# Kernel tuning notes

Hardware: AMD Instinct MI355X
Metric: run time of the kernel (lower is better)

The kernel has to match this reference:

```python
import jax, jax.numpy as jnp
import numpy as np

N, V, E = 65536, 2048, 1024
TEMPERATURE = 0.5
EPS = 1e-10
LOG_PARAM_Q = -2.995732273553991


def _l2_normalize(x, axis):
    # matches torch F.normalize(p=2): x / max(||x||, 1e-12)
    n = jnp.sqrt(jnp.sum(x * x, axis=axis, keepdims=True))
    return x / jnp.maximum(n, 1e-12)


def setup_inputs() -> dict:
    key = jax.random.key(0)
    k1, k2, k3 = jax.random.split(key, 3)
    z = jax.random.normal(k1, (N, E), dtype=jnp.float32)
    emb_weight = jax.random.normal(k2, (V, E), dtype=jnp.float32)
    U = jax.random.uniform(k3, (N, V), dtype=jnp.float32)
    return {"z": z, "emb_weight": emb_weight, "U": U}


def reference(z, emb_weight, U):
    kappa_q = jnp.exp(jnp.float32(LOG_PARAM_Q)) + jnp.float32(1.0)
    zn = _l2_normalize(z, axis=1)              # [N, E]
    emb = _l2_normalize(emb_weight, axis=1)    # [V, E]
    # logit = -distances = kappa_q * z @ emb.T
    logit = kappa_q * jnp.matmul(zn, emb.T)    # [N, V]
    # gumbel-softmax sample (training branch)
    g = -jnp.log(-jnp.log(U + EPS) + EPS)
    tokens = jax.nn.softmax((logit + g) / TEMPERATURE, axis=-1)  # [N, V]
    z_q = jnp.matmul(tokens, emb)              # [N, E]
    return (tokens, z_q)
```

## Files before the change

### kernel.cpp

```cpp
#include <hip/hip_runtime.h>
#include <hip/hip_bf16.h>
#include <stdint.h>

typedef short bf16x8 __attribute__((ext_vector_type(8)));
typedef float floatx4 __attribute__((ext_vector_type(4)));

#define N_ROWS 65536
#define V_DIM 2048
#define E_DIM 1024

__device__ __forceinline__ short f2bf(float x) {
  union { float f; uint32_t u; } c; c.f = x;
  uint32_t r = (c.u + 0x7FFFu + ((c.u >> 16) & 1u)) >> 16;
  return (short)(uint16_t)r;
}
__device__ __forceinline__ float bf16f(short b) {
  union { uint32_t u; float f; } c; c.u = ((uint32_t)(uint16_t)b) << 16;
  return c.f;
}

__device__ __forceinline__ float wave_sum(float v) {
#pragma unroll
  for (int o = 32; o > 0; o >>= 1) v += __shfl_xor(v, o);
  return v;
}
__device__ __forceinline__ float wave_max(float v) {
#pragma unroll
  for (int o = 32; o > 0; o >>= 1) v = fmaxf(v, __shfl_xor(v, o));
  return v;
}

__device__ __forceinline__ void gll16(const short* g, short* l) {
  __builtin_amdgcn_global_load_lds(
      (const __attribute__((address_space(1))) void*)g,
      (__attribute__((address_space(3))) void*)l, 16, 0, 0);
}

#define FRAG(base, R, c) \
  (*(const bf16x8*)((const char*)(base) + ((R) << 7) + (((((c) >> 3) ^ ((R) & 7))) << 4)))

__global__ __launch_bounds__(256) void k_norm_emb(const float* __restrict__ W,
                                                  short* __restrict__ embn,
                                                  short* __restrict__ embnT) {
  const int v = blockIdx.x;
  const int t = threadIdx.x;
  const int w = t >> 6, l = t & 63;
  const float4 val = *(const float4*)&W[(size_t)v * E_DIM + t * 4];
  float ss = val.x * val.x + val.y * val.y + val.z * val.z + val.w * val.w;
  ss = wave_sum(ss);
  __shared__ float red[4];
  if (l == 0) red[w] = ss;
  __syncthreads();
  ss = red[0] + red[1] + red[2] + red[3];
  const float inv = 1.0f / fmaxf(sqrtf(ss), 1e-12f);
  short4 o;
  o.x = f2bf(val.x * inv);
  o.y = f2bf(val.y * inv);
  o.z = f2bf(val.z * inv);
  o.w = f2bf(val.w * inv);
  *(short4*)&embn[(size_t)v * E_DIM + t * 4] = o;
  embnT[(size_t)(t * 4 + 0) * V_DIM + v] = o.x;
  embnT[(size_t)(t * 4 + 1) * V_DIM + v] = o.y;
  embnT[(size_t)(t * 4 + 2) * V_DIM + v] = o.z;
  embnT[(size_t)(t * 4 + 3) * V_DIM + v] = o.w;
}

__global__ __launch_bounds__(256) void k_norm_z(const float* __restrict__ Z,
                                                short* __restrict__ zn) {
  const int w = threadIdx.x >> 6, l = threadIdx.x & 63;
  const int row = blockIdx.x * 4 + w;
  const float* zr = Z + (size_t)row * E_DIM;
  float4 v[4];
  float ss = 0.f;
#pragma unroll
  for (int i = 0; i < 4; ++i) {
    v[i] = *(const float4*)&zr[(i * 64 + l) * 4];
    ss += v[i].x * v[i].x + v[i].y * v[i].y + v[i].z * v[i].z + v[i].w * v[i].w;
  }
  ss = wave_sum(ss);
  const float SCALE = 2.0f * (expf(-2.995732273553991f) + 1.0f);
  const float inv = SCALE / fmaxf(sqrtf(ss), 1e-12f);
  short* zo = zn + (size_t)row * E_DIM;
#pragma unroll
  for (int i = 0; i < 4; ++i) {
    short4 o;
    o.x = f2bf(v[i].x * inv);
    o.y = f2bf(v[i].y * inv);
    o.z = f2bf(v[i].z * inv);
    o.w = f2bf(v[i].w * inv);
    *(short4*)&zo[(i * 64 + l) * 4] = o;
  }
}

template <int KDIM, int NBX, int EPI>
__global__ __launch_bounds__(512, 2) void k_gemm8(
    const short* __restrict__ A, const short* __restrict__ B,
    const float* __restrict__ U, short* __restrict__ Pb,
    float* __restrict__ partials, const float* __restrict__ invsum,
    float* __restrict__ C, int cpx) {
  __shared__ __align__(16) short Sm[65536];
  const int NT = KDIM / 32;
  const int tid = threadIdx.x;
  const int wv = tid >> 6, lane = tid & 63;
  const int lr = lane & 15, lh = lane >> 4;
  const int wr = wv >> 2, wc = wv & 3;
  const int d = blockIdx.x;
  const int L = (d & 7) * cpx + (d >> 3);
  const int by = L / NBX, bx = L % NBX;
  const int m0 = by * 256, n0 = bx * 256;
  const int sg = (((lane & 3) ^ ((lane >> 2) & 3) ^ ((lane >> 4) & 3)) << 3);
  const int srow = wv * 16 + (lane >> 2);
  const short* gA = A + (size_t)(m0 + srow) * KDIM + sg;
  const short* gB = B + (size_t)(n0 + srow) * KDIM + sg;
  const int fslot = lh ^ ((lr ^ (lr >> 2)) & 3);
  const int aoff = wr * 8192 + lr * 64 + fslot * 16;
  const int boff = wc * 4096 + lr * 64 + fslot * 16;

  bf16x8 af[4], afN[4], bfr[4];
  floatx4 acc[8][4] = {};

#define STAGE(KT)                                                                   \
  {                                                                                 \
    short* An_ = Sm + ((KT) & 3) * 8192;                                            \
    short* Bn_ = Sm + 32768 + ((KT) & 3) * 8192;                                    \
    const size_t kc_ = (size_t)(KT) * 32;                                           \
    gll16(gA + kc_, An_ + wv * 512);                                                \
    gll16(gA + (size_t)128 * KDIM + kc_, An_ + 4096 + wv * 512);                    \
    gll16(gB + kc_, Bn_ + wv * 512);                                                \
    gll16(gB + (size_t)128 * KDIM + kc_, Bn_ + 4096 + wv * 512);                    \
  }
#define RD_B(KT)                                                                    \
  {                                                                                 \
    const char* Bb_ = (const char*)Sm + 65536 + ((KT) & 3) * 16384;                 \
    _Pragma("unroll")                                                               \
    for (int n = 0; n < 4; ++n) bfr[n] = *(const bf16x8*)(Bb_ + boff + n * 1024);   \
  }
#define RD_ALO(KT)                                                                  \
  {                                                                                 \
    const char* Ab_ = (const char*)Sm + ((KT) & 3) * 16384;                         \
    _Pragma("unroll")                                                               \
    for (int i = 0; i < 4; ++i) af[i] = *(const bf16x8*)(Ab_ + aoff + i * 1024);    \
  }
#define RD_AHI(KT)                                                                  \
  {                                                                                 \
    const char* Ab_ = (const char*)Sm + ((KT) & 3) * 16384;                         \
    _Pragma("unroll")                                                               \
    for (int i = 0; i < 4; ++i)                                                     \
      afN[i] = *(const bf16x8*)(Ab_ + aoff + 4096 + i * 1024);                      \
  }
#define MF_LO                                                                       \
  __builtin_amdgcn_s_setprio(1);                                                    \
  _Pragma("unroll")                                                                 \
  for (int i = 0; i < 4; ++i) {                                                     \
    _Pragma("unroll")                                                               \
    for (int n = 0; n < 4; ++n)                                                     \
      acc[i][n] = __builtin_amdgcn_mfma_f32_16x16x32_bf16(af[i], bfr[n], acc[i][n], 0, 0, 0); \
  }                                                                                 \
  __builtin_amdgcn_s_setprio(0);
#define MF_HI                                                                       \
  __builtin_amdgcn_s_setprio(1);                                                    \
  _Pragma("unroll")                                                                 \
  for (int i = 0; i < 4; ++i) {                                                     \
    _Pragma("unroll")                                                               \
    for (int n = 0; n < 4; ++n)                                                     \
      acc[4 + i][n] = __builtin_amdgcn_mfma_f32_16x16x32_bf16(afN[i], bfr[n], acc[4 + i][n], 0, 0, 0); \
  }                                                                                 \
  __builtin_amdgcn_s_setprio(0);

  STAGE(0);
  STAGE(1);
  asm volatile("s_waitcnt vmcnt(4)" ::: "memory");
  __builtin_amdgcn_s_barrier();
  __builtin_amdgcn_sched_barrier(0);
  RD_B(0);
  RD_ALO(0);

#pragma unroll 2
  for (int kt = 0; kt < NT - 2; ++kt) {
    STAGE(kt + 2);
    RD_AHI(kt);
    MF_LO;
    MF_HI;
    asm volatile("s_waitcnt vmcnt(4)" ::: "memory");
    __builtin_amdgcn_s_barrier();
    __builtin_amdgcn_sched_barrier(0);
    RD_B(kt + 1);
    RD_ALO(kt + 1);
  }
  RD_AHI(NT - 2);
  MF_LO;
  MF_HI;
  asm volatile("s_waitcnt vmcnt(0)" ::: "memory");
  __builtin_amdgcn_s_barrier();
  __builtin_amdgcn_sched_barrier(0);
  RD_B(NT - 1);
  RD_ALO(NT - 1);
  RD_AHI(NT - 1);
  MF_LO;
  MF_HI;
#undef STAGE
#undef RD_B
#undef RD_ALO
#undef RD_AHI
#undef MF_LO
#undef MF_HI

  const int gr0 = m0 + wr * 128 + lh * 4;
  const int gc0 = n0 + wc * 64 + lr;
  if (EPI == 0) {
    float rs[8][4] = {};
#pragma unroll
    for (int m = 0; m < 8; ++m)
#pragma unroll
      for (int n = 0; n < 4; ++n) {
        const int col = gc0 + n * 16;
#pragma unroll
        for (int j = 0; j < 4; ++j) {
          const int row = gr0 + m * 16 + j;
          const size_t idx = (size_t)row * V_DIM + col;
          const float u = U[idx];
          const float e = __expf(acc[m][n][j] - 2.f * __logf(-__logf(u + 1e-10f) + 1e-10f));
          const short eb = f2bf(e);
          Pb[idx] = eb;
          rs[m][j] += bf16f(eb);
        }
      }
#pragma unroll
    for (int m = 0; m < 8; ++m)
#pragma unroll
      for (int j = 0; j < 4; ++j) {
        float s = rs[m][j];
        s += __shfl_xor(s, 1); s += __shfl_xor(s, 2);
        s += __shfl_xor(s, 4); s += __shfl_xor(s, 8);
        if (lr == 0)
          partials[(size_t)(gr0 + m * 16 + j) * 32 + bx * 4 + wc] = s;
      }
  } else {
#pragma unroll
    for (int m = 0; m < 8; ++m)
#pragma unroll
      for (int j = 0; j < 4; ++j) {
        const int row = gr0 + m * 16 + j;
        const float s = invsum[row];
#pragma unroll
        for (int n = 0; n < 4; ++n)
          C[(size_t)row * E_DIM + gc0 + n * 16] = acc[m][n][j] * s;
      }
  }
}

__global__ __launch_bounds__(256) void k_rowsum_inv(const float* __restrict__ partials,
                                                    float* __restrict__ invsum) {
  const int r = blockIdx.x * 256 + threadIdx.x;
  const float4* p = (const float4*)&partials[(size_t)r * 32];
  float s = 0.f;
#pragma unroll
  for (int i = 0; i < 8; ++i) { float4 v = p[i]; s += v.x + v.y + v.z + v.w; }
  invsum[r] = 1.f / s;
}

__global__ __launch_bounds__(256) void k_token_norm(const short* __restrict__ Pb,
                                                    const float* __restrict__ invsum,
                                                    float* __restrict__ tokens) {
  const size_t stride = (size_t)gridDim.x * 256 * 8;
  for (size_t i = ((size_t)blockIdx.x * 256 + threadIdx.x) * 8;
       i < (size_t)N_ROWS * V_DIM; i += stride) {
    const float s = invsum[i >> 11];
    const bf16x8 v = *(const bf16x8*)&Pb[i];
    float4 o0, o1;
    o0.x = bf16f(v[0]) * s; o0.y = bf16f(v[1]) * s;
    o0.z = bf16f(v[2]) * s; o0.w = bf16f(v[3]) * s;
    o1.x = bf16f(v[4]) * s; o1.y = bf16f(v[5]) * s;
    o1.z = bf16f(v[6]) * s; o1.w = bf16f(v[7]) * s;
    *(float4*)&tokens[i] = o0;
    *(float4*)&tokens[i + 4] = o1;
  }
}

__global__ __launch_bounds__(256) void k_gemm_nt(const short* __restrict__ A,
                                                 const short* __restrict__ B,
                                                 float* __restrict__ C,
                                                 int lda, int ldb, int ldc, int K) {
  __shared__ __align__(16) short As[128][64];
  __shared__ __align__(16) short Bs[128][64];
  const int t = threadIdx.x;
  const int w = t >> 6, l = t & 63;
  const int lr = l & 15, lh = l >> 4;
  const int m0 = blockIdx.y * 128, n0 = blockIdx.x * 128;
  const int wm = (w >> 1) * 64, wn = (w & 1) * 64;
  floatx4 acc[4][4] = {};
  for (int k0 = 0; k0 < K; k0 += 64) {
    __syncthreads();
#pragma unroll
    for (int i = 0; i < 4; ++i) {
      const int c = i * 256 + t;
      const int r = c >> 3, c8 = (c & 7) * 8;
      *(bf16x8*)&As[r][c8] = *(const bf16x8*)&A[(size_t)(m0 + r) * lda + k0 + c8];
      *(bf16x8*)&Bs[r][c8] = *(const bf16x8*)&B[(size_t)(n0 + r) * ldb + k0 + c8];
    }
    __syncthreads();
#pragma unroll
    for (int kk = 0; kk < 64; kk += 32) {
      bf16x8 af[4], bfr[4];
#pragma unroll
      for (int m = 0; m < 4; ++m) af[m] = *(const bf16x8*)&As[wm + m * 16 + lr][kk + lh * 8];
#pragma unroll
      for (int n = 0; n < 4; ++n) bfr[n] = *(const bf16x8*)&Bs[wn + n * 16 + lr][kk + lh * 8];
#pragma unroll
      for (int m = 0; m < 4; ++m)
#pragma unroll
        for (int n = 0; n < 4; ++n)
          acc[m][n] = __builtin_amdgcn_mfma_f32_16x16x32_bf16(af[m], bfr[n], acc[m][n], 0, 0, 0);
    }
  }
#pragma unroll
  for (int m = 0; m < 4; ++m)
#pragma unroll
    for (int n = 0; n < 4; ++n) {
      const int col = n0 + wn + n * 16 + lr;
#pragma unroll
      for (int j = 0; j < 4; ++j)
        C[(size_t)(m0 + wm + m * 16 + lh * 4 + j) * ldc + col] = acc[m][n][j];
    }
}

__global__ __launch_bounds__(256) void k_gemm_nt_f32a(const float* __restrict__ A,
                                                      const short* __restrict__ B,
                                                      float* __restrict__ C,
                                                      int lda, int ldb, int ldc, int K) {
  __shared__ __align__(16) short As[128][64];
  __shared__ __align__(16) short Bs[128][64];
  const int t = threadIdx.x;
  const int w = t >> 6, l = t & 63;
  const int lr = l & 15, lh = l >> 4;
  const int m0 = blockIdx.y * 128, n0 = blockIdx.x * 128;
  const int wm = (w >> 1) * 64, wn = (w & 1) * 64;
  floatx4 acc[4][4] = {};
  for (int k0 = 0; k0 < K; k0 += 64) {
    __syncthreads();
#pragma unroll
    for (int i = 0; i < 4; ++i) {
      const int c = i * 256 + t;
      const int r = c >> 3, c8 = (c & 7) * 8;
      const float4 a0 = *(const float4*)&A[(size_t)(m0 + r) * lda + k0 + c8];
      const float4 a1 = *(const float4*)&A[(size_t)(m0 + r) * lda + k0 + c8 + 4];
      bf16x8 va;
      va[0] = f2bf(a0.x); va[1] = f2bf(a0.y); va[2] = f2bf(a0.z); va[3] = f2bf(a0.w);
      va[4] = f2bf(a1.x); va[5] = f2bf(a1.y); va[6] = f2bf(a1.z); va[7] = f2bf(a1.w);
      *(bf16x8*)&As[r][c8] = va;
      *(bf16x8*)&Bs[r][c8] = *(const bf16x8*)&B[(size_t)(n0 + r) * ldb + k0 + c8];
    }
    __syncthreads();
#pragma unroll
    for (int kk = 0; kk < 64; kk += 32) {
      bf16x8 af[4], bfr[4];
#pragma unroll
      for (int m = 0; m < 4; ++m) af[m] = *(const bf16x8*)&As[wm + m * 16 + lr][kk + lh * 8];
#pragma unroll
      for (int n = 0; n < 4; ++n) bfr[n] = *(const bf16x8*)&Bs[wn + n * 16 + lr][kk + lh * 8];
#pragma unroll
      for (int m = 0; m < 4; ++m)
#pragma unroll
        for (int n = 0; n < 4; ++n)
          acc[m][n] = __builtin_amdgcn_mfma_f32_16x16x32_bf16(af[m], bfr[n], acc[m][n], 0, 0, 0);
    }
  }
#pragma unroll
  for (int m = 0; m < 4; ++m)
#pragma unroll
    for (int n = 0; n < 4; ++n) {
      const int col = n0 + wn + n * 16 + lr;
#pragma unroll
      for (int j = 0; j < 4; ++j)
        C[(size_t)(m0 + wm + m * 16 + lh * 4 + j) * ldc + col] = acc[m][n][j];
    }
}

__global__ __launch_bounds__(256) void k_gumbel_softmax(float* __restrict__ S,
                                                        const float* __restrict__ U) {
  const int t = threadIdx.x;
  const int w = t >> 6, l = t & 63;
  const size_t base = (size_t)blockIdx.x * V_DIM + t * 8;
  const float4 s0 = *(const float4*)&S[base];
  const float4 s1 = *(const float4*)&S[base + 4];
  const float4 u0 = *(const float4*)&U[base];
  const float4 u1 = *(const float4*)&U[base + 4];
  float x[8];
  x[0] = s0.x - 2.f * __logf(-__logf(u0.x + 1e-10f) + 1e-10f);
  x[1] = s0.y - 2.f * __logf(-__logf(u0.y + 1e-10f) + 1e-10f);
  x[2] = s0.z - 2.f * __logf(-__logf(u0.z + 1e-10f) + 1e-10f);
  x[3] = s0.w - 2.f * __logf(-__logf(u0.w + 1e-10f) + 1e-10f);
  x[4] = s1.x - 2.f * __logf(-__logf(u1.x + 1e-10f) + 1e-10f);
  x[5] = s1.y - 2.f * __logf(-__logf(u1.y + 1e-10f) + 1e-10f);
  x[6] = s1.z - 2.f * __logf(-__logf(u1.z + 1e-10f) + 1e-10f);
  x[7] = s1.w - 2.f * __logf(-__logf(u1.w + 1e-10f) + 1e-10f);
  float lm = x[0];
#pragma unroll
  for (int i = 1; i < 8; ++i) lm = fmaxf(lm, x[i]);
  lm = wave_max(lm);
  __shared__ float redA[4], redB[4];
  if (l == 0) redA[w] = lm;
  __syncthreads();
  const float m = fmaxf(fmaxf(redA[0], redA[1]), fmaxf(redA[2], redA[3]));
  float p[8];
  float ls = 0.f;
#pragma unroll
  for (int i = 0; i < 8; ++i) { p[i] = __expf(x[i] - m); ls += p[i]; }
  ls = wave_sum(ls);
  if (l == 0) redB[w] = ls;
  __syncthreads();
  const float inv = 1.0f / (redB[0] + redB[1] + redB[2] + redB[3]);
  float4 o0 = make_float4(p[0] * inv, p[1] * inv, p[2] * inv, p[3] * inv);
  float4 o1 = make_float4(p[4] * inv, p[5] * inv, p[6] * inv, p[7] * inv);
  *(float4*)&S[base] = o0;
  *(float4*)&S[base + 4] = o1;
}

extern "C" void kernel_launch(void* const* d_in, const int* in_sizes, int n_in,
                              void* d_out, int out_size, void* d_ws, size_t ws_size,
                              hipStream_t stream) {
  const float* z = (const float*)d_in[0];
  const float* W = (const float*)d_in[1];
  const float* U = (const float*)d_in[2];
  float* tokens = (float*)d_out;
  float* zq = tokens + (size_t)N_ROWS * V_DIM;
  short* zn = (short*)zq;

  short* embn = (short*)d_ws;
  short* embnT = embn + (size_t)V_DIM * E_DIM;

  const size_t NEED = (size_t)V_DIM * E_DIM * 2 * 2
                    + (size_t)N_ROWS * 32 * 4
                    + (size_t)N_ROWS * 4
                    + (size_t)N_ROWS * V_DIM * 2;

  k_norm_emb<<<V_DIM, 256, 0, stream>>>(W, embn, embnT);
  k_norm_z<<<N_ROWS / 4, 256, 0, stream>>>(z, zn);

  if (ws_size >= NEED) {
    float* partials = (float*)(embnT + (size_t)V_DIM * E_DIM);
    float* invsum = partials + (size_t)N_ROWS * 32;
    short* Pb = (short*)(invsum + N_ROWS);
    k_gemm8<E_DIM, 8, 0><<<2048, 512, 0, stream>>>(
        zn, embn, U, Pb, partials, nullptr, nullptr, 2048 / 8);
    k_rowsum_inv<<<N_ROWS / 256, 256, 0, stream>>>(partials, invsum);
    k_token_norm<<<2048, 256, 0, stream>>>(Pb, invsum, tokens);
    k_gemm8<V_DIM, 4, 1><<<1024, 512, 0, stream>>>(
        Pb, embnT, nullptr, nullptr, nullptr, invsum, zq, 1024 / 8);
  } else {
    k_gemm_nt<<<dim3(V_DIM / 128, N_ROWS / 128), 256, 0, stream>>>(
        zn, embn, tokens, E_DIM, E_DIM, V_DIM, E_DIM);
    k_gumbel_softmax<<<N_ROWS, 256, 0, stream>>>(tokens, U);
    k_gemm_nt_f32a<<<dim3(E_DIM / 128, N_ROWS / 128), 256, 0, stream>>>(
        tokens, embnT, zq, V_DIM, V_DIM, E_DIM, V_DIM);
  }
}
```

Measured before the change: 1.013 ms.

## Fuse token normalization into second GEMM and prefetch U for epilogue

```diff
diff --git a/kernel.cpp b/kernel.cpp
--- a/kernel.cpp
+++ b/kernel.cpp
@@ -97,7 +97,7 @@
     const short* __restrict__ A, const short* __restrict__ B,
     const float* __restrict__ U, short* __restrict__ Pb,
     float* __restrict__ partials, const float* __restrict__ invsum,
-    float* __restrict__ C, int cpx) {
+    float* __restrict__ C, float* __restrict__ tokens, int cpx) {
   __shared__ __align__(16) short Sm[65536];
   const int NT = KDIM / 32;
   const int tid = threadIdx.x;
@@ -116,8 +116,31 @@
   const int aoff = wr * 8192 + lr * 64 + fslot * 16;
   const int boff = wc * 4096 + lr * 64 + fslot * 16;
 
+  const int gr0 = m0 + wr * 128 + lh * 4;
+  const int gc0 = n0 + wc * 64 + lr;
+  const float* Ug = U + (size_t)gr0 * V_DIM + gc0;
+
+  float inv0 = 0.f, inv1 = 0.f;
+  if (EPI == 1) {
+    inv0 = invsum[m0 + srow];
+    inv1 = invsum[m0 + 128 + srow];
+  }
+
   bf16x8 af[4], afN[4], bfr[4];
   floatx4 acc[8][4] = {};
+  float u01[32], u23[32];
+
+#define UPREF(arr, P)                                                               \
+  {                                                                                 \
+    _Pragma("unroll")                                                               \
+    for (int mm = 0; mm < 2; ++mm)                                                  \
+      _Pragma("unroll")                                                             \
+      for (int n = 0; n < 4; ++n)                                                   \
+        _Pragma("unroll")                                                           \
+        for (int j = 0; j < 4; ++j)                                                 \
+          arr[mm * 16 + n * 4 + j] =                                                \
+              Ug[(size_t)(((2 * (P) + mm) * 16 + j)) * V_DIM + n * 16];             \
+  }
 
 #define STAGE(KT)                                                                   \
   {                                                                                 \
@@ -166,6 +189,26 @@
       acc[4 + i][n] = __builtin_amdgcn_mfma_f32_16x16x32_bf16(afN[i], bfr[n], acc[4 + i][n], 0, 0, 0); \
   }                                                                                 \
   __builtin_amdgcn_s_setprio(0);
+#define TOKW(KT)                                                                    \
+  if (EPI == 1 && ((KT) >> 4) == bx) {                                              \
+    const short* myA_ = Sm + ((KT) & 3) * 8192 + wv * 512 + lane * 8;               \
+    const bf16x8 v0_ = *(const bf16x8*)myA_;                                        \
+    const bf16x8 v1_ = *(const bf16x8*)(myA_ + 4096);                               \
+    const size_t c0_ = (size_t)(KT) * 32 + sg;                                      \
+    float4 a_, b_;                                                                  \
+    a_.x = bf16f(v0_[0]) * inv0; a_.y = bf16f(v0_[1]) * inv0;                       \
+    a_.z = bf16f(v0_[2]) * inv0; a_.w = bf16f(v0_[3]) * inv0;                       \
+    b_.x = bf16f(v0_[4]) * inv0; b_.y = bf16f(v0_[5]) * inv0;                       \
+    b_.z = bf16f(v0_[6]) * inv0; b_.w = bf16f(v0_[7]) * inv0;                       \
+    *(float4*)&tokens[(size_t)(m0 + srow) * KDIM + c0_] = a_;                       \
+    *(float4*)&tokens[(size_t)(m0 + srow) * KDIM + c0_ + 4] = b_;                   \
+    a_.x = bf16f(v1_[0]) * inv1; a_.y = bf16f(v1_[1]) * inv1;                       \
+    a_.z = bf16f(v1_[2]) * inv1; a_.w = bf16f(v1_[3]) * inv1;                       \
+    b_.x = bf16f(v1_[4]) * inv1; b_.y = bf16f(v1_[5]) * inv1;                       \
+    b_.z = bf16f(v1_[6]) * inv1; b_.w = bf16f(v1_[7]) * inv1;                       \
+    *(float4*)&tokens[(size_t)(m0 + 128 + srow) * KDIM + c0_] = a_;                 \
+    *(float4*)&tokens[(size_t)(m0 + 128 + srow) * KDIM + c0_ + 4] = b_;             \
+  }
 
   STAGE(0);
   STAGE(1);
@@ -177,10 +220,13 @@
 
 #pragma unroll 2
   for (int kt = 0; kt < NT - 2; ++kt) {
+    if (EPI == 0 && kt == NT - 6) UPREF(u01, 0);
+    if (EPI == 0 && kt == NT - 4) UPREF(u23, 1);
     STAGE(kt + 2);
     RD_AHI(kt);
     MF_LO;
     MF_HI;
+    TOKW(kt);
     asm volatile("s_waitcnt vmcnt(4)" ::: "memory");
     __builtin_amdgcn_s_barrier();
     __builtin_amdgcn_sched_barrier(0);
@@ -190,6 +236,7 @@
   RD_AHI(NT - 2);
   MF_LO;
   MF_HI;
+  TOKW(NT - 2);
   asm volatile("s_waitcnt vmcnt(0)" ::: "memory");
   __builtin_amdgcn_s_barrier();
   __builtin_amdgcn_sched_barrier(0);
@@ -198,33 +245,45 @@
   RD_AHI(NT - 1);
   MF_LO;
   MF_HI;
+  TOKW(NT - 1);
 #undef STAGE
 #undef RD_B
 #undef RD_ALO
 #undef RD_AHI
 #undef MF_LO
 #undef MF_HI
-
-  const int gr0 = m0 + wr * 128 + lh * 4;
-  const int gc0 = n0 + wc * 64 + lr;
+#undef TOKW
+
   if (EPI == 0) {
     float rs[8][4] = {};
-#pragma unroll
-    for (int m = 0; m < 8; ++m)
-#pragma unroll
-      for (int n = 0; n < 4; ++n) {
-        const int col = gc0 + n * 16;
-#pragma unroll
-        for (int j = 0; j < 4; ++j) {
-          const int row = gr0 + m * 16 + j;
-          const size_t idx = (size_t)row * V_DIM + col;
-          const float u = U[idx];
-          const float e = __expf(acc[m][n][j] - 2.f * __logf(-__logf(u + 1e-10f) + 1e-10f));
-          const short eb = f2bf(e);
-          Pb[idx] = eb;
-          rs[m][j] += bf16f(eb);
-        }
-      }
+    float u45[32], u67[32];
+    UPREF(u45, 2);
+#define EPI_PAIR(P, arr)                                                            \
+    _Pragma("unroll")                                                               \
+    for (int mm = 0; mm < 2; ++mm) {                                                \
+      const int m = 2 * (P) + mm;                                                   \
+      _Pragma("unroll")                                                             \
+      for (int n = 0; n < 4; ++n) {                                                 \
+        const int col = gc0 + n * 16;                                               \
+        _Pragma("unroll")                                                           \
+        for (int j = 0; j < 4; ++j) {                                               \
+          const int row = gr0 + m * 16 + j;                                         \
+          const size_t idx = (size_t)row * V_DIM + col;                             \
+          const float u = arr[mm * 16 + n * 4 + j];                                 \
+          const float e = __expf(acc[m][n][j] -                                     \
+                                 2.f * __logf(-__logf(u + 1e-10f) + 1e-10f));       \
+          const short eb = f2bf(e);                                                 \
+          Pb[idx] = eb;                                                             \
+          rs[m][j] += bf16f(eb);                                                    \
+        }                                                                           \
+      }                                                                             \
+    }
+    EPI_PAIR(0, u01);
+    UPREF(u67, 3);
+    EPI_PAIR(1, u23);
+    EPI_PAIR(2, u45);
+    EPI_PAIR(3, u67);
+#undef EPI_PAIR
 #pragma unroll
     for (int m = 0; m < 8; ++m)
 #pragma unroll
@@ -247,6 +306,7 @@
           C[(size_t)row * E_DIM + gc0 + n * 16] = acc[m][n][j] * s;
       }
   }
+#undef UPREF
 }
 
 __global__ __launch_bounds__(256) void k_rowsum_inv(const float* __restrict__ partials,
@@ -257,24 +317,6 @@
 #pragma unroll
   for (int i = 0; i < 8; ++i) { float4 v = p[i]; s += v.x + v.y + v.z + v.w; }
   invsum[r] = 1.f / s;
-}
-
-__global__ __launch_bounds__(256) void k_token_norm(const short* __restrict__ Pb,
-                                                    const float* __restrict__ invsum,
-                                                    float* __restrict__ tokens) {
-  const size_t stride = (size_t)gridDim.x * 256 * 8;
-  for (size_t i = ((size_t)blockIdx.x * 256 + threadIdx.x) * 8;
-       i < (size_t)N_ROWS * V_DIM; i += stride) {
-    const float s = invsum[i >> 11];
-    const bf16x8 v = *(const bf16x8*)&Pb[i];
-    float4 o0, o1;
-    o0.x = bf16f(v[0]) * s; o0.y = bf16f(v[1]) * s;
-    o0.z = bf16f(v[2]) * s; o0.w = bf16f(v[3]) * s;
-    o1.x = bf16f(v[4]) * s; o1.y = bf16f(v[5]) * s;
-    o1.z = bf16f(v[6]) * s; o1.w = bf16f(v[7]) * s;
-    *(float4*)&tokens[i] = o0;
-    *(float4*)&tokens[i + 4] = o1;
-  }
 }
 
 __global__ __launch_bounds__(256) void k_gemm_nt(const short* __restrict__ A,
@@ -442,11 +484,10 @@
     float* invsum = partials + (size_t)N_ROWS * 32;
     short* Pb = (short*)(invsum + N_ROWS);
     k_gemm8<E_DIM, 8, 0><<<2048, 512, 0, stream>>>(
-        zn, embn, U, Pb, partials, nullptr, nullptr, 2048 / 8);
+        zn, embn, U, Pb, partials, nullptr, nullptr, nullptr, 2048 / 8);
     k_rowsum_inv<<<N_ROWS / 256, 256, 0, stream>>>(partials, invsum);
-    k_token_norm<<<2048, 256, 0, stream>>>(Pb, invsum, tokens);
     k_gemm8<V_DIM, 4, 1><<<1024, 512, 0, stream>>>(
-        Pb, embnT, nullptr, nullptr, nullptr, invsum, zq, 1024 / 8);
+        Pb, embnT, nullptr, nullptr, nullptr, invsum, zq, tokens, 1024 / 8);
   } else {
     k_gemm_nt<<<dim3(V_DIM / 128, N_ROWS / 128), 256, 0, stream>>>(
         zn, embn, tokens, E_DIM, E_DIM, V_DIM, E_DIM);
```

New measurement: 1.425 ms. +40.7%, slower.
